# Performance work log

Hardware: AMD Instinct MI355X
Metric: run time of the kernel (lower is better)

The kernel has to match this reference:

```python
import jax, jax.numpy as jnp
import numpy as np

N, E, D_IN, D_H, D_OUT = 50000, 640000, 128, 128, 64
EPS = 1e-5


def _sage(x, src, dst, Wl, bl, Wr):
    # PyG SAGEConv: out = lin_l(mean_{j in N(i)} x_j) + lin_r(x_i)
    msg = x[src]                                             # [E, d] gather
    agg = jax.ops.segment_sum(msg, dst, num_segments=x.shape[0])
    deg = jax.ops.segment_sum(jnp.ones((src.shape[0],), x.dtype), dst,
                              num_segments=x.shape[0])
    agg = agg / jnp.maximum(deg, 1.0)[:, None]               # mean aggregate
    return agg @ Wl + bl + x @ Wr


def _bn_eval(x, gamma, beta, mean, var):
    return (x - mean) * jax.lax.rsqrt(var + EPS) * gamma + beta


def setup_inputs() -> dict:
    key = jax.random.key(0)
    ks = jax.random.split(key, 16)
    s = lambda d: 1.0 / np.sqrt(d)
    inp = {
        "x": jax.random.normal(ks[0], (N, D_IN), jnp.float32),
        "edge_index": jax.random.randint(ks[1], (2, E), 0, N, jnp.int64),
        # layer 0: 128 -> 128
        "Wl0": jax.random.normal(ks[2], (D_IN, D_H), jnp.float32) * s(D_IN),
        "bl0": jnp.zeros((D_H,), jnp.float32),
        "Wr0": jax.random.normal(ks[3], (D_IN, D_H), jnp.float32) * s(D_IN),
        # layer 1: 128 -> 128
        "Wl1": jax.random.normal(ks[4], (D_H, D_H), jnp.float32) * s(D_H),
        "bl1": jnp.zeros((D_H,), jnp.float32),
        "Wr1": jax.random.normal(ks[5], (D_H, D_H), jnp.float32) * s(D_H),
        # layer 2: 128 -> 64
        "Wl2": jax.random.normal(ks[6], (D_H, D_OUT), jnp.float32) * s(D_H),
        "bl2": jnp.zeros((D_OUT,), jnp.float32),
        "Wr2": jax.random.normal(ks[7], (D_H, D_OUT), jnp.float32) * s(D_H),
        # BatchNorm (eval mode) for the two hidden layers
        "g0": jnp.ones((D_H,), jnp.float32),
        "b0": jnp.zeros((D_H,), jnp.float32),
        "m0": jax.random.normal(ks[8], (D_H,), jnp.float32) * 0.1,
        "v0": jax.random.uniform(ks[9], (D_H,), jnp.float32, 0.5, 1.5),
        "g1": jnp.ones((D_H,), jnp.float32),
        "b1": jnp.zeros((D_H,), jnp.float32),
        "m1": jax.random.normal(ks[10], (D_H,), jnp.float32) * 0.1,
        "v1": jax.random.uniform(ks[11], (D_H,), jnp.float32, 0.5, 1.5),
    }
    return inp


def reference(x, edge_index, Wl0, bl0, Wr0, Wl1, bl1, Wr1, Wl2, bl2, Wr2,
              g0, b0, m0, v0, g1, b1, m1, v1):
    src, dst = edge_index[0], edge_index[1]
    # edge mask (edge_index < N) is all-true by construction -> no-op
    h = _sage(x, src, dst, Wl0, bl0, Wr0)
    h = jax.nn.relu(_bn_eval(h, g0, b0, m0, v0))   # eval: dropout is identity
    h = _sage(h, src, dst, Wl1, bl1, Wr1)
    h = jax.nn.relu(_bn_eval(h, g1, b1, m1, v1))
    h = _sage(h, src, dst, Wl2, bl2, Wr2)
    return jax.nn.log_softmax(h, axis=1)
```

## Files before the change

kernel.cpp:

```cpp
#include <hip/hip_runtime.h>

#define EPS 1e-5f
#define ELL_CAP 64

typedef __attribute__((ext_vector_type(8))) short short8;
typedef __attribute__((ext_vector_type(4))) float f32x4;

__device__ inline unsigned short f2b(float f) {
    union { float f; unsigned u; } v; v.f = f;
    unsigned u = v.u;
    return (unsigned short)((u + 0x7fffu + ((u >> 16) & 1u)) >> 16);
}
__device__ inline float b2f(unsigned short u) {
    union { unsigned u; float f; } v;
    v.u = ((unsigned)u) << 16;
    return v.f;
}


__device__ inline void cvt_one(const float* Wl, const float* Wr,
                               unsigned short* BT, int dout, int idx) {
    int n = idx >> 7, k = idx & 127;
    float w = (n < dout) ? Wl[k * dout + n] : Wr[k * dout + (n - dout)];
    BT[idx] = f2b(w);
}

__global__ void k_cvt_w3(const float* __restrict__ Wl0, const float* __restrict__ Wr0,
                         const float* __restrict__ Wl1, const float* __restrict__ Wr1,
                         const float* __restrict__ Wl2, const float* __restrict__ Wr2,
                         unsigned short* __restrict__ BT0,
                         unsigned short* __restrict__ BT1,
                         unsigned short* __restrict__ BT2,
                         int* __restrict__ cnt, int N) {
    int idx = blockIdx.x * blockDim.x + threadIdx.x;
    const int S0 = 256 * 128, S1 = 256 * 128, S2 = 128 * 128;
    if (idx < N) cnt[idx] = 0;
    if (idx < S0) cvt_one(Wl0, Wr0, BT0, 128, idx);
    else if (idx < S0 + S1) cvt_one(Wl1, Wr1, BT1, 128, idx - S0);
    else if (idx < S0 + S1 + S2) cvt_one(Wl2, Wr2, BT2, 64, idx - S0 - S1);
}


__global__ void k_build_ell(const int* __restrict__ src, const int* __restrict__ dst,
                            int E, int* __restrict__ cnt,
                            unsigned short* __restrict__ ell) {
    int i = blockIdx.x * blockDim.x + threadIdx.x;
    int T = gridDim.x * blockDim.x;
    int e0 = i, e1 = i + T, e2 = i + 2 * T, e3 = i + 3 * T;
    int d0 = 0, d1 = 0, d2 = 0, d3 = 0;
    int s0 = 0, s1 = 0, s2 = 0, s3 = 0;
    if (e0 < E) { d0 = dst[e0]; s0 = src[e0]; }
    if (e1 < E) { d1 = dst[e1]; s1 = src[e1]; }
    if (e2 < E) { d2 = dst[e2]; s2 = src[e2]; }
    if (e3 < E) { d3 = dst[e3]; s3 = src[e3]; }
    int p0 = 0, p1 = 0, p2 = 0, p3 = 0;
    if (e0 < E) p0 = atomicAdd(&cnt[d0], 1);
    if (e1 < E) p1 = atomicAdd(&cnt[d1], 1);
    if (e2 < E) p2 = atomicAdd(&cnt[d2], 1);
    if (e3 < E) p3 = atomicAdd(&cnt[d3], 1);
    if (e0 < E && p0 < ELL_CAP) ell[(size_t)d0 * ELL_CAP + p0] = (unsigned short)s0;
    if (e1 < E && p1 < ELL_CAP) ell[(size_t)d1 * ELL_CAP + p1] = (unsigned short)s1;
    if (e2 < E && p2 < ELL_CAP) ell[(size_t)d2 * ELL_CAP + p2] = (unsigned short)s2;
    if (e3 < E && p3 < ELL_CAP) ell[(size_t)d3 * ELL_CAP + p3] = (unsigned short)s3;
}


__device__ inline short8 pack8(float4 a, float4 b) {
    short8 r;
    r[0] = (short)f2b(a.x); r[1] = (short)f2b(a.y);
    r[2] = (short)f2b(a.z); r[3] = (short)f2b(a.w);
    r[4] = (short)f2b(b.x); r[5] = (short)f2b(b.y);
    r[6] = (short)f2b(b.z); r[7] = (short)f2b(b.w);
    return r;
}

template <int NCOLS, bool A32>
__global__ void k_mgemm_lds(const void* __restrict__ Av,
                            const unsigned short* __restrict__ BT,
                            unsigned short* __restrict__ C,
                            int M) {
    __shared__ __align__(16) unsigned short Bs[8 * 4 * 64 * 8];

    const int tid  = threadIdx.x;
    const int lane = tid & 63;
    const int wave = tid >> 6;
    const int m16  = lane & 15;
    const int q    = lane >> 4;
    const int row0 = (blockIdx.x * 4 + wave) * 16;
    const int col0 = blockIdx.y * 128;

#pragma unroll
    for (int i = 0; i < 8; ++i) {
        int f   = tid + i * 256;
        int t   = f >> 8;
        int kc  = (f >> 6) & 3;
        int ln  = f & 63;
        int bm  = ln & 15, bq = ln >> 4;
        const short8* gp = (const short8*)(BT + (size_t)(col0 + t * 16 + bm) * 128
                                              + kc * 32 + bq * 8);
        *(short8*)(Bs + (size_t)f * 8) = *gp;
    }

    int arow = row0 + m16;
    if (arow >= M) arow = M - 1;
    short8 af0, af1, af2, af3;
    if (A32) {
        const float4* Ap = (const float4*)((const float*)Av + (size_t)arow * 128 + q * 8);
        af0 = pack8(Ap[0],  Ap[1]);
        af1 = pack8(Ap[8],  Ap[9]);
        af2 = pack8(Ap[16], Ap[17]);
        af3 = pack8(Ap[24], Ap[25]);
    } else {
        const short8* Ap = (const short8*)((const unsigned short*)Av + (size_t)arow * 128 + q * 8);
        af0 = Ap[0]; af1 = Ap[4]; af2 = Ap[8]; af3 = Ap[12];
    }

    __syncthreads();

    f32x4 acc[8] = {};
#pragma unroll
    for (int t = 0; t < 8; ++t) {
        const short8* bp = (const short8*)(Bs + (size_t)(t * 4) * 64 * 8 + (size_t)lane * 8);
        short8 b0 = bp[0];
        short8 b1 = bp[64];
        short8 b2 = bp[128];
        short8 b3 = bp[192];
        acc[t] = __builtin_amdgcn_mfma_f32_16x16x32_bf16(af0, b0, acc[t], 0, 0, 0);
        acc[t] = __builtin_amdgcn_mfma_f32_16x16x32_bf16(af1, b1, acc[t], 0, 0, 0);
        acc[t] = __builtin_amdgcn_mfma_f32_16x16x32_bf16(af2, b2, acc[t], 0, 0, 0);
        acc[t] = __builtin_amdgcn_mfma_f32_16x16x32_bf16(af3, b3, acc[t], 0, 0, 0);
    }

#pragma unroll
    for (int r = 0; r < 4; ++r) {
        int row = row0 + q * 4 + r;
        if (row < M) {
            unsigned short* cp = C + (size_t)row * NCOLS + col0 + m16;
#pragma unroll
            for (int t = 0; t < 8; ++t) cp[t * 16] = f2b(acc[t][r]);
        }
    }
}


__global__ void k_agg128(const unsigned short* __restrict__ PQ,
                         const int* __restrict__ cnt,
                         const unsigned short* __restrict__ ell,
                         const float* __restrict__ bl,
                         const float* __restrict__ g, const float* __restrict__ b,
                         const float* __restrict__ m, const float* __restrict__ v,
                         unsigned short* __restrict__ out, int n) {
    int node = (blockIdx.x * blockDim.x + threadIdx.x) >> 6;
    int lane = threadIdx.x & 63;
    if (node >= n) return;
    int cn  = cnt[node];
    int deg = min(cn, ELL_CAP);
    int myidx = (lane < deg) ? (int)ell[(size_t)node * ELL_CAP + lane] : 0;
    const int half = lane >> 5, hl = lane & 31;

    float a0 = 0.f, a1 = 0.f, a2 = 0.f, a3 = 0.f;
    int j = 0;
    for (; j + 4 <= deg; j += 4) {
        int ia = __shfl(myidx, j + half);
        int ib = __shfl(myidx, j + 2 + half);
        ushort4 pa = *(const ushort4*)(PQ + (size_t)ia * 256 + 4 * hl);
        ushort4 pb = *(const ushort4*)(PQ + (size_t)ib * 256 + 4 * hl);
        a0 += b2f(pa.x) + b2f(pb.x);
        a1 += b2f(pa.y) + b2f(pb.y);
        a2 += b2f(pa.z) + b2f(pb.z);
        a3 += b2f(pa.w) + b2f(pb.w);
    }
    for (; j < deg; j += 2) {
        int rem = deg - j;
        int ia = __shfl(myidx, min(j + half, deg - 1));
        if (half == 0 || rem >= 2) {
            ushort4 pa = *(const ushort4*)(PQ + (size_t)ia * 256 + 4 * hl);
            a0 += b2f(pa.x); a1 += b2f(pa.y); a2 += b2f(pa.z); a3 += b2f(pa.w);
        }
    }
    a0 += __shfl_xor(a0, 32);
    a1 += __shfl_xor(a1, 32);
    a2 += __shfl_xor(a2, 32);
    a3 += __shfl_xor(a3, 32);

    float dg = fmaxf((float)cn, 1.f);
    ushort4 qv = *(const ushort4*)(PQ + (size_t)node * 256 + 128 + 4 * hl);
    int c0 = 4 * hl;
    float4 blv = *(const float4*)(bl + c0);
    float4 mv  = *(const float4*)(m + c0);
    float4 vv  = *(const float4*)(v + c0);
    float4 gv  = *(const float4*)(g + c0);
    float4 bv  = *(const float4*)(b + c0);
    float z0 = (a0 / dg + b2f(qv.x) + blv.x - mv.x) * rsqrtf(vv.x + EPS) * gv.x + bv.x;
    float z1 = (a1 / dg + b2f(qv.y) + blv.y - mv.y) * rsqrtf(vv.y + EPS) * gv.y + bv.y;
    float z2 = (a2 / dg + b2f(qv.z) + blv.z - mv.z) * rsqrtf(vv.z + EPS) * gv.z + bv.z;
    float z3 = (a3 / dg + b2f(qv.w) + blv.w - mv.w) * rsqrtf(vv.w + EPS) * gv.w + bv.w;
    if (half == 0) {
        ushort4 r;
        r.x = f2b(fmaxf(z0, 0.f));
        r.y = f2b(fmaxf(z1, 0.f));
        r.z = f2b(fmaxf(z2, 0.f));
        r.w = f2b(fmaxf(z3, 0.f));
        *(ushort4*)(out + (size_t)node * 128 + c0) = r;
    }
}


__global__ void k_agg64(const unsigned short* __restrict__ PQ,
                        const int* __restrict__ cnt,
                        const unsigned short* __restrict__ ell,
                        const float* __restrict__ bl,
                        float* __restrict__ out, int n) {
    int node = (blockIdx.x * blockDim.x + threadIdx.x) >> 6;
    int lane = threadIdx.x & 63;
    if (node >= n) return;
    int cn  = cnt[node];
    int deg = min(cn, ELL_CAP);
    int myidx = (lane < deg) ? (int)ell[(size_t)node * ELL_CAP + lane] : 0;
    const int qtr = lane >> 4, ql = lane & 15;

    float a0 = 0.f, a1 = 0.f, a2 = 0.f, a3 = 0.f;
    int j = 0;
    for (; j + 8 <= deg; j += 8) {
        int ia = __shfl(myidx, j + qtr);
        int ib = __shfl(myidx, j + 4 + qtr);
        ushort4 pa = *(const ushort4*)(PQ + (size_t)ia * 128 + 4 * ql);
        ushort4 pb = *(const ushort4*)(PQ + (size_t)ib * 128 + 4 * ql);
        a0 += b2f(pa.x) + b2f(pb.x);
        a1 += b2f(pa.y) + b2f(pb.y);
        a2 += b2f(pa.z) + b2f(pb.z);
        a3 += b2f(pa.w) + b2f(pb.w);
    }
    for (; j < deg; j += 4) {
        int rem = deg - j;
        int ia = __shfl(myidx, min(j + qtr, deg - 1));
        if (qtr < rem) {
            ushort4 pa = *(const ushort4*)(PQ + (size_t)ia * 128 + 4 * ql);
            a0 += b2f(pa.x); a1 += b2f(pa.y); a2 += b2f(pa.z); a3 += b2f(pa.w);
        }
    }
    a0 += __shfl_xor(a0, 16); a0 += __shfl_xor(a0, 32);
    a1 += __shfl_xor(a1, 16); a1 += __shfl_xor(a1, 32);
    a2 += __shfl_xor(a2, 16); a2 += __shfl_xor(a2, 32);
    a3 += __shfl_xor(a3, 16); a3 += __shfl_xor(a3, 32);

    float dg = fmaxf((float)cn, 1.f);
    ushort4 qv = *(const ushort4*)(PQ + (size_t)node * 128 + 64 + 4 * ql);
    int c0 = 4 * ql;
    float4 blv = *(const float4*)(bl + c0);
    float z0 = a0 / dg + b2f(qv.x) + blv.x;
    float z1 = a1 / dg + b2f(qv.y) + blv.y;
    float z2 = a2 / dg + b2f(qv.z) + blv.z;
    float z3 = a3 / dg + b2f(qv.w) + blv.w;

    float mx = fmaxf(fmaxf(z0, z1), fmaxf(z2, z3));
#pragma unroll
    for (int off = 8; off > 0; off >>= 1) mx = fmaxf(mx, __shfl_xor(mx, off));
    float sm = __expf(z0 - mx) + __expf(z1 - mx) + __expf(z2 - mx) + __expf(z3 - mx);
#pragma unroll
    for (int off = 8; off > 0; off >>= 1) sm += __shfl_xor(sm, off);
    float lg = mx + __logf(sm);
    if (qtr == 0) {
        float4 o = make_float4(z0 - lg, z1 - lg, z2 - lg, z3 - lg);
        *(float4*)(out + (size_t)node * 64 + c0) = o;
    }
}


extern "C" void kernel_launch(void* const* d_in, const int* in_sizes, int n_in,
                              void* d_out, int out_size, void* d_ws, size_t ws_size,
                              hipStream_t stream) {
    const float* x   = (const float*)d_in[0];
    const int*   ei  = (const int*)d_in[1];
    const float* Wl0 = (const float*)d_in[2];
    const float* bl0 = (const float*)d_in[3];
    const float* Wr0 = (const float*)d_in[4];
    const float* Wl1 = (const float*)d_in[5];
    const float* bl1 = (const float*)d_in[6];
    const float* Wr1 = (const float*)d_in[7];
    const float* Wl2 = (const float*)d_in[8];
    const float* bl2 = (const float*)d_in[9];
    const float* Wr2 = (const float*)d_in[10];
    const float* g0  = (const float*)d_in[11];
    const float* b0  = (const float*)d_in[12];
    const float* m0  = (const float*)d_in[13];
    const float* v0  = (const float*)d_in[14];
    const float* g1  = (const float*)d_in[15];
    const float* b1  = (const float*)d_in[16];
    const float* m1  = (const float*)d_in[17];
    const float* v1  = (const float*)d_in[18];

    const int N = in_sizes[0] / 128;
    const int E = in_sizes[1] / 2;
    const int* src = ei;
    const int* dst = ei + E;

    size_t off = 0;
    auto alloc = [&](size_t bytes) -> void* {
        void* p = (char*)d_ws + off;
        off += (bytes + 255) & ~(size_t)255;
        return p;
    };
    int* cnt = (int*)alloc((size_t)N * 4);
    unsigned short* ell = (unsigned short*)alloc((size_t)N * ELL_CAP * 2);
    unsigned short* PQ  = (unsigned short*)alloc((size_t)N * 256 * 2);
    unsigned short* hb  = (unsigned short*)alloc((size_t)N * 128 * 2);
    unsigned short* BT0 = (unsigned short*)alloc((size_t)256 * 128 * 2);
    unsigned short* BT1 = (unsigned short*)alloc((size_t)256 * 128 * 2);
    unsigned short* BT2 = (unsigned short*)alloc((size_t)128 * 128 * 2);
    (void)ws_size;

    const int CVT_TOTAL = 256 * 128 + 256 * 128 + 128 * 128;
    k_cvt_w3<<<(CVT_TOTAL + 255) / 256, 256, 0, stream>>>(
        Wl0, Wr0, Wl1, Wr1, Wl2, Wr2, BT0, BT1, BT2, cnt, N);

    int buildThreads = (E + 3) / 4;
    k_build_ell<<<(buildThreads + 255) / 256, 256, 0, stream>>>(src, dst, E, cnt, ell);

    int rowBlocks = (N + 63) / 64;
    dim3 mg2(rowBlocks, 2);
    dim3 mg1(rowBlocks, 1);
    int aggGrid = (N + 3) / 4;

    k_mgemm_lds<256, true><<<mg2, 256, 0, stream>>>(x, BT0, PQ, N);
    k_agg128<<<aggGrid, 256, 0, stream>>>(PQ, cnt, ell, bl0, g0, b0, m0, v0, hb, N);
    k_mgemm_lds<256, false><<<mg2, 256, 0, stream>>>(hb, BT1, PQ, N);
    k_agg128<<<aggGrid, 256, 0, stream>>>(PQ, cnt, ell, bl1, g1, b1, m1, v1, hb, N);
    k_mgemm_lds<128, false><<<mg1, 256, 0, stream>>>(hb, BT2, PQ, N);
    k_agg64<<<aggGrid, 256, 0, stream>>>(PQ, cnt, ell, bl2, (float*)d_out, N);
}
```

Measured before the change: 268.2 us.

## Fuse ELL build with first GEMM in one launch and pad atomic counters

Merges the edge-list ELL construction and the layer-0 feature GEMM into a single kernel whose blocks are split by index: the first blocks build the ELL and the rest run the GEMM, so the two independent phases can overlap on the GPU. Per-node degree counters are padded to a 16-int stride to spread atomics across cache lines, and they are now zeroed with a memset instead of inside the weight-conversion kernel. The padding makes the counter array 16x larger and scatters the degree reads in the aggregation kernels. The merged kernel also carries the GEMM's LDS allocation in the build blocks, which may limit their occupancy.

```diff
diff --git a/kernel.cpp b/kernel.cpp
--- a/kernel.cpp
+++ b/kernel.cpp
@@ -2,6 +2,7 @@
 
 #define EPS 1e-5f
 #define ELL_CAP 64
+#define CNT_STRIDE 16
 
 typedef __attribute__((ext_vector_type(8))) short short8;
 typedef __attribute__((ext_vector_type(4))) float f32x4;
@@ -30,38 +31,12 @@
                          const float* __restrict__ Wl2, const float* __restrict__ Wr2,
                          unsigned short* __restrict__ BT0,
                          unsigned short* __restrict__ BT1,
-                         unsigned short* __restrict__ BT2,
-                         int* __restrict__ cnt, int N) {
+                         unsigned short* __restrict__ BT2) {
     int idx = blockIdx.x * blockDim.x + threadIdx.x;
     const int S0 = 256 * 128, S1 = 256 * 128, S2 = 128 * 128;
-    if (idx < N) cnt[idx] = 0;
     if (idx < S0) cvt_one(Wl0, Wr0, BT0, 128, idx);
     else if (idx < S0 + S1) cvt_one(Wl1, Wr1, BT1, 128, idx - S0);
     else if (idx < S0 + S1 + S2) cvt_one(Wl2, Wr2, BT2, 64, idx - S0 - S1);
-}
-
-
-__global__ void k_build_ell(const int* __restrict__ src, const int* __restrict__ dst,
-                            int E, int* __restrict__ cnt,
-                            unsigned short* __restrict__ ell) {
-    int i = blockIdx.x * blockDim.x + threadIdx.x;
-    int T = gridDim.x * blockDim.x;
-    int e0 = i, e1 = i + T, e2 = i + 2 * T, e3 = i + 3 * T;
-    int d0 = 0, d1 = 0, d2 = 0, d3 = 0;
-    int s0 = 0, s1 = 0, s2 = 0, s3 = 0;
-    if (e0 < E) { d0 = dst[e0]; s0 = src[e0]; }
-    if (e1 < E) { d1 = dst[e1]; s1 = src[e1]; }
-    if (e2 < E) { d2 = dst[e2]; s2 = src[e2]; }
-    if (e3 < E) { d3 = dst[e3]; s3 = src[e3]; }
-    int p0 = 0, p1 = 0, p2 = 0, p3 = 0;
-    if (e0 < E) p0 = atomicAdd(&cnt[d0], 1);
-    if (e1 < E) p1 = atomicAdd(&cnt[d1], 1);
-    if (e2 < E) p2 = atomicAdd(&cnt[d2], 1);
-    if (e3 < E) p3 = atomicAdd(&cnt[d3], 1);
-    if (e0 < E && p0 < ELL_CAP) ell[(size_t)d0 * ELL_CAP + p0] = (unsigned short)s0;
-    if (e1 < E && p1 < ELL_CAP) ell[(size_t)d1 * ELL_CAP + p1] = (unsigned short)s1;
-    if (e2 < E && p2 < ELL_CAP) ell[(size_t)d2 * ELL_CAP + p2] = (unsigned short)s2;
-    if (e3 < E && p3 < ELL_CAP) ell[(size_t)d3 * ELL_CAP + p3] = (unsigned short)s3;
 }
 
 
@@ -75,19 +50,18 @@
 }
 
 template <int NCOLS, bool A32>
-__global__ void k_mgemm_lds(const void* __restrict__ Av,
-                            const unsigned short* __restrict__ BT,
-                            unsigned short* __restrict__ C,
-                            int M) {
-    __shared__ __align__(16) unsigned short Bs[8 * 4 * 64 * 8];
-
+__device__ inline void gemm_body(unsigned short* Bs,
+                                 const void* __restrict__ Av,
+                                 const unsigned short* __restrict__ BT,
+                                 unsigned short* __restrict__ C,
+                                 int M, int bx, int by) {
     const int tid  = threadIdx.x;
     const int lane = tid & 63;
     const int wave = tid >> 6;
     const int m16  = lane & 15;
     const int q    = lane >> 4;
-    const int row0 = (blockIdx.x * 4 + wave) * 16;
-    const int col0 = blockIdx.y * 128;
+    const int row0 = (bx * 4 + wave) * 16;
+    const int col0 = by * 128;
 
 #pragma unroll
     for (int i = 0; i < 8; ++i) {
@@ -142,6 +116,48 @@
     }
 }
 
+template <int NCOLS, bool A32>
+__global__ void k_mgemm_lds(const void* __restrict__ Av,
+                            const unsigned short* __restrict__ BT,
+                            unsigned short* __restrict__ C, int M) {
+    __shared__ __align__(16) unsigned short Bs[8 * 4 * 64 * 8];
+    gemm_body<NCOLS, A32>(Bs, Av, BT, C, M, blockIdx.x, blockIdx.y);
+}
+
+
+__global__ void k_mega(const int* __restrict__ src, const int* __restrict__ dst,
+                       int E, int* __restrict__ cnt, unsigned short* __restrict__ ell,
+                       int buildBlocks,
+                       const float* __restrict__ x,
+                       const unsigned short* __restrict__ BT0,
+                       unsigned short* __restrict__ PQ, int M) {
+    __shared__ __align__(16) unsigned short Bs[8 * 4 * 64 * 8];
+
+    if ((int)blockIdx.x < buildBlocks) {
+        int i = blockIdx.x * blockDim.x + threadIdx.x;
+        int T = buildBlocks * blockDim.x;
+        int e0 = i, e1 = i + T, e2 = i + 2 * T, e3 = i + 3 * T;
+        int d0 = 0, d1 = 0, d2 = 0, d3 = 0;
+        int s0 = 0, s1 = 0, s2 = 0, s3 = 0;
+        if (e0 < E) { d0 = dst[e0]; s0 = src[e0]; }
+        if (e1 < E) { d1 = dst[e1]; s1 = src[e1]; }
+        if (e2 < E) { d2 = dst[e2]; s2 = src[e2]; }
+        if (e3 < E) { d3 = dst[e3]; s3 = src[e3]; }
+        int p0 = 0, p1 = 0, p2 = 0, p3 = 0;
+        if (e0 < E) p0 = atomicAdd(&cnt[(size_t)d0 * CNT_STRIDE], 1);
+        if (e1 < E) p1 = atomicAdd(&cnt[(size_t)d1 * CNT_STRIDE], 1);
+        if (e2 < E) p2 = atomicAdd(&cnt[(size_t)d2 * CNT_STRIDE], 1);
+        if (e3 < E) p3 = atomicAdd(&cnt[(size_t)d3 * CNT_STRIDE], 1);
+        if (e0 < E && p0 < ELL_CAP) ell[(size_t)d0 * ELL_CAP + p0] = (unsigned short)s0;
+        if (e1 < E && p1 < ELL_CAP) ell[(size_t)d1 * ELL_CAP + p1] = (unsigned short)s1;
+        if (e2 < E && p2 < ELL_CAP) ell[(size_t)d2 * ELL_CAP + p2] = (unsigned short)s2;
+        if (e3 < E && p3 < ELL_CAP) ell[(size_t)d3 * ELL_CAP + p3] = (unsigned short)s3;
+        return;
+    }
+    int bid = blockIdx.x - buildBlocks;
+    gemm_body<256, true>(Bs, x, BT0, PQ, M, bid >> 1, bid & 1);
+}
+
 
 __global__ void k_agg128(const unsigned short* __restrict__ PQ,
                          const int* __restrict__ cnt,
@@ -153,7 +169,7 @@
     int node = (blockIdx.x * blockDim.x + threadIdx.x) >> 6;
     int lane = threadIdx.x & 63;
     if (node >= n) return;
-    int cn  = cnt[node];
+    int cn  = cnt[(size_t)node * CNT_STRIDE];
     int deg = min(cn, ELL_CAP);
     int myidx = (lane < deg) ? (int)ell[(size_t)node * ELL_CAP + lane] : 0;
     const int half = lane >> 5, hl = lane & 31;
@@ -214,7 +230,7 @@
     int node = (blockIdx.x * blockDim.x + threadIdx.x) >> 6;
     int lane = threadIdx.x & 63;
     if (node >= n) return;
-    int cn  = cnt[node];
+    int cn  = cnt[(size_t)node * CNT_STRIDE];
     int deg = min(cn, ELL_CAP);
     int myidx = (lane < deg) ? (int)ell[(size_t)node * ELL_CAP + lane] : 0;
     const int qtr = lane >> 4, ql = lane & 15;
@@ -301,7 +317,7 @@
         off += (bytes + 255) & ~(size_t)255;
         return p;
     };
-    int* cnt = (int*)alloc((size_t)N * 4);
+    int* cnt = (int*)alloc((size_t)N * CNT_STRIDE * 4);
     unsigned short* ell = (unsigned short*)alloc((size_t)N * ELL_CAP * 2);
     unsigned short* PQ  = (unsigned short*)alloc((size_t)N * 256 * 2);
     unsigned short* hb  = (unsigned short*)alloc((size_t)N * 128 * 2);
@@ -310,19 +326,21 @@
     unsigned short* BT2 = (unsigned short*)alloc((size_t)128 * 128 * 2);
     (void)ws_size;
 
+    hipMemsetAsync(cnt, 0, (size_t)N * CNT_STRIDE * 4, stream);
     const int CVT_TOTAL = 256 * 128 + 256 * 128 + 128 * 128;
     k_cvt_w3<<<(CVT_TOTAL + 255) / 256, 256, 0, stream>>>(
-        Wl0, Wr0, Wl1, Wr1, Wl2, Wr2, BT0, BT1, BT2, cnt, N);
-
-    int buildThreads = (E + 3) / 4;
-    k_build_ell<<<(buildThreads + 255) / 256, 256, 0, stream>>>(src, dst, E, cnt, ell);
+        Wl0, Wr0, Wl1, Wr1, Wl2, Wr2, BT0, BT1, BT2);
 
     int rowBlocks = (N + 63) / 64;
     dim3 mg2(rowBlocks, 2);
     dim3 mg1(rowBlocks, 1);
     int aggGrid = (N + 3) / 4;
 
-    k_mgemm_lds<256, true><<<mg2, 256, 0, stream>>>(x, BT0, PQ, N);
+    int buildBlocks = ((E + 3) / 4 + 255) / 256;
+    int gemmBlocks  = rowBlocks * 2;
+    k_mega<<<buildBlocks + gemmBlocks, 256, 0, stream>>>(
+        src, dst, E, cnt, ell, buildBlocks, x, BT0, PQ, N);
+
     k_agg128<<<aggGrid, 256, 0, stream>>>(PQ, cnt, ell, bl0, g0, b0, m0, v0, hb, N);
     k_mgemm_lds<256, false><<<mg2, 256, 0, stream>>>(hb, BT1, PQ, N);
     k_agg128<<<aggGrid, 256, 0, stream>>>(PQ, cnt, ell, bl1, g1, b1, m1, v1, hb, N);
```

Measured after the change: 261.4 us. 1.03x faster.

## Store neighbor projections in FP8 and fuse ELL build with first GEMM

Applied to the files above, without the earlier changes.

The neighbor-side projection (P) of layers 0 and 1 is now written as FP8 in its own buffer, while the self projection (Q) stays bf16 in a separate buffer. This halves the bytes the gather-heavy aggregation kernels read per edge. The ELL adjacency build is also merged into the first GEMM launch as extra blocks, so the two can run concurrently and one launch is saved. The cost is lower precision in the aggregated messages, which may hurt accuracy. The fused kernel also adds a grid-stride edge loop over a fixed number of build blocks.

```diff
diff --git a/kernel.cpp b/kernel.cpp
--- a/kernel.cpp
+++ b/kernel.cpp
@@ -2,9 +2,12 @@
 
 #define EPS 1e-5f
 #define ELL_CAP 64
+#define BLK 256
+#define BUILD_BLOCKS 128
 
 typedef __attribute__((ext_vector_type(8))) short short8;
 typedef __attribute__((ext_vector_type(4))) float f32x4;
+typedef __attribute__((ext_vector_type(2))) float f32x2;
 
 __device__ inline unsigned short f2b(float f) {
     union { float f; unsigned u; } v; v.f = f;
@@ -15,6 +18,10 @@
     union { unsigned u; float f; } v;
     v.u = ((unsigned)u) << 16;
     return v.f;
+}
+__device__ inline unsigned char f2p8(float f) {
+    int pk = __builtin_amdgcn_cvt_pk_fp8_f32(f, f, 0, false);
+    return (unsigned char)(pk & 0xff);
 }
 
 
@@ -25,43 +32,19 @@
     BT[idx] = f2b(w);
 }
 
-__global__ void k_cvt_w3(const float* __restrict__ Wl0, const float* __restrict__ Wr0,
-                         const float* __restrict__ Wl1, const float* __restrict__ Wr1,
-                         const float* __restrict__ Wl2, const float* __restrict__ Wr2,
-                         unsigned short* __restrict__ BT0,
-                         unsigned short* __restrict__ BT1,
-                         unsigned short* __restrict__ BT2,
-                         int* __restrict__ cnt, int N) {
+__global__ void k_prep(const float* __restrict__ Wl0, const float* __restrict__ Wr0,
+                       const float* __restrict__ Wl1, const float* __restrict__ Wr1,
+                       const float* __restrict__ Wl2, const float* __restrict__ Wr2,
+                       unsigned short* __restrict__ BT0,
+                       unsigned short* __restrict__ BT1,
+                       unsigned short* __restrict__ BT2,
+                       int* __restrict__ cnt, int N) {
     int idx = blockIdx.x * blockDim.x + threadIdx.x;
+    if (idx < N) cnt[idx] = 0;
     const int S0 = 256 * 128, S1 = 256 * 128, S2 = 128 * 128;
-    if (idx < N) cnt[idx] = 0;
     if (idx < S0) cvt_one(Wl0, Wr0, BT0, 128, idx);
     else if (idx < S0 + S1) cvt_one(Wl1, Wr1, BT1, 128, idx - S0);
     else if (idx < S0 + S1 + S2) cvt_one(Wl2, Wr2, BT2, 64, idx - S0 - S1);
-}
-
-
-__global__ void k_build_ell(const int* __restrict__ src, const int* __restrict__ dst,
-                            int E, int* __restrict__ cnt,
-                            unsigned short* __restrict__ ell) {
-    int i = blockIdx.x * blockDim.x + threadIdx.x;
-    int T = gridDim.x * blockDim.x;
-    int e0 = i, e1 = i + T, e2 = i + 2 * T, e3 = i + 3 * T;
-    int d0 = 0, d1 = 0, d2 = 0, d3 = 0;
-    int s0 = 0, s1 = 0, s2 = 0, s3 = 0;
-    if (e0 < E) { d0 = dst[e0]; s0 = src[e0]; }
-    if (e1 < E) { d1 = dst[e1]; s1 = src[e1]; }
-    if (e2 < E) { d2 = dst[e2]; s2 = src[e2]; }
-    if (e3 < E) { d3 = dst[e3]; s3 = src[e3]; }
-    int p0 = 0, p1 = 0, p2 = 0, p3 = 0;
-    if (e0 < E) p0 = atomicAdd(&cnt[d0], 1);
-    if (e1 < E) p1 = atomicAdd(&cnt[d1], 1);
-    if (e2 < E) p2 = atomicAdd(&cnt[d2], 1);
-    if (e3 < E) p3 = atomicAdd(&cnt[d3], 1);
-    if (e0 < E && p0 < ELL_CAP) ell[(size_t)d0 * ELL_CAP + p0] = (unsigned short)s0;
-    if (e1 < E && p1 < ELL_CAP) ell[(size_t)d1 * ELL_CAP + p1] = (unsigned short)s1;
-    if (e2 < E && p2 < ELL_CAP) ell[(size_t)d2 * ELL_CAP + p2] = (unsigned short)s2;
-    if (e3 < E && p3 < ELL_CAP) ell[(size_t)d3 * ELL_CAP + p3] = (unsigned short)s3;
 }
 
 
@@ -74,20 +57,21 @@
     return r;
 }
 
-template <int NCOLS, bool A32>
-__global__ void k_mgemm_lds(const void* __restrict__ Av,
-                            const unsigned short* __restrict__ BT,
-                            unsigned short* __restrict__ C,
-                            int M) {
-    __shared__ __align__(16) unsigned short Bs[8 * 4 * 64 * 8];
-
+template <int NCOLS, bool A32, int OUT>
+__device__ inline void gemm_tile(unsigned short* Bs,
+                                 const void* __restrict__ Av,
+                                 const unsigned short* __restrict__ BT,
+                                 unsigned short* __restrict__ C,
+                                 unsigned char* __restrict__ P8,
+                                 unsigned short* __restrict__ Qb,
+                                 int M, int bx, int by) {
     const int tid  = threadIdx.x;
     const int lane = tid & 63;
     const int wave = tid >> 6;
     const int m16  = lane & 15;
     const int q    = lane >> 4;
-    const int row0 = (blockIdx.x * 4 + wave) * 16;
-    const int col0 = blockIdx.y * 128;
+    const int row0 = (bx * 4 + wave) * 16;
+    const int col0 = by * 128;
 
 #pragma unroll
     for (int i = 0; i < 8; ++i) {
@@ -135,15 +119,79 @@
     for (int r = 0; r < 4; ++r) {
         int row = row0 + q * 4 + r;
         if (row < M) {
-            unsigned short* cp = C + (size_t)row * NCOLS + col0 + m16;
-#pragma unroll
-            for (int t = 0; t < 8; ++t) cp[t * 16] = f2b(acc[t][r]);
+            if (OUT == 0) {
+                unsigned short* cp = C + (size_t)row * NCOLS + col0 + m16;
+#pragma unroll
+                for (int t = 0; t < 8; ++t) cp[t * 16] = f2b(acc[t][r]);
+            } else if (by == 0) {
+                unsigned char* cp = P8 + (size_t)row * 128 + m16;
+#pragma unroll
+                for (int t = 0; t < 8; ++t) cp[t * 16] = f2p8(acc[t][r]);
+            } else {
+                unsigned short* cp = Qb + (size_t)row * 128 + m16;
+#pragma unroll
+                for (int t = 0; t < 8; ++t) cp[t * 16] = f2b(acc[t][r]);
+            }
         }
     }
-}
-
-
-__global__ void k_agg128(const unsigned short* __restrict__ PQ,
+    __syncthreads();
+}
+
+
+__global__ void k_mega(const int* __restrict__ src, const int* __restrict__ dst,
+                       int E, int* __restrict__ cnt, unsigned short* __restrict__ ell,
+                       const float* __restrict__ x,
+                       const unsigned short* __restrict__ BT0,
+                       unsigned char* __restrict__ P8,
+                       unsigned short* __restrict__ Qb, int M) {
+    __shared__ __align__(16) unsigned short Bs[8 * 4 * 64 * 8];
+
+    if ((int)blockIdx.x < BUILD_BLOCKS) {
+        const int T = BUILD_BLOCKS * BLK;
+        int i = blockIdx.x * BLK + threadIdx.x;
+        for (int base = 0; base < E; base += 4 * T) {
+            int e0 = base + i, e1 = e0 + T, e2 = e1 + T, e3 = e2 + T;
+            int d0 = 0, d1 = 0, d2 = 0, d3 = 0;
+            int s0 = 0, s1 = 0, s2 = 0, s3 = 0;
+            if (e0 < E) { d0 = dst[e0]; s0 = src[e0]; }
+            if (e1 < E) { d1 = dst[e1]; s1 = src[e1]; }
+            if (e2 < E) { d2 = dst[e2]; s2 = src[e2]; }
+            if (e3 < E) { d3 = dst[e3]; s3 = src[e3]; }
+            int p0 = 0, p1 = 0, p2 = 0, p3 = 0;
+            if (e0 < E) p0 = atomicAdd(&cnt[d0], 1);
+            if (e1 < E) p1 = atomicAdd(&cnt[d1], 1);
+            if (e2 < E) p2 = atomicAdd(&cnt[d2], 1);
+            if (e3 < E) p3 = atomicAdd(&cnt[d3], 1);
+            if (e0 < E && p0 < ELL_CAP) ell[(size_t)d0 * ELL_CAP + p0] = (unsigned short)s0;
+            if (e1 < E && p1 < ELL_CAP) ell[(size_t)d1 * ELL_CAP + p1] = (unsigned short)s1;
+            if (e2 < E && p2 < ELL_CAP) ell[(size_t)d2 * ELL_CAP + p2] = (unsigned short)s2;
+            if (e3 < E && p3 < ELL_CAP) ell[(size_t)d3 * ELL_CAP + p3] = (unsigned short)s3;
+        }
+        return;
+    }
+    int bid = blockIdx.x - BUILD_BLOCKS;
+    gemm_tile<256, true, 1>(Bs, x, BT0, nullptr, P8, Qb, M, bid >> 1, bid & 1);
+}
+
+
+__global__ void k_gemm1(const unsigned short* __restrict__ A,
+                        const unsigned short* __restrict__ BT,
+                        unsigned char* __restrict__ P8,
+                        unsigned short* __restrict__ Qb, int M) {
+    __shared__ __align__(16) unsigned short Bs[8 * 4 * 64 * 8];
+    gemm_tile<256, false, 1>(Bs, A, BT, nullptr, P8, Qb, M, blockIdx.x, blockIdx.y);
+}
+
+__global__ void k_gemm2(const unsigned short* __restrict__ A,
+                        const unsigned short* __restrict__ BT,
+                        unsigned short* __restrict__ C, int M) {
+    __shared__ __align__(16) unsigned short Bs[8 * 4 * 64 * 8];
+    gemm_tile<128, false, 0>(Bs, A, BT, C, nullptr, nullptr, M, blockIdx.x, 0);
+}
+
+
+__global__ void k_agg128(const unsigned char* __restrict__ P8,
+                         const unsigned short* __restrict__ Qb,
                          const int* __restrict__ cnt,
                          const unsigned short* __restrict__ ell,
                          const float* __restrict__ bl,
@@ -163,19 +211,25 @@
     for (; j + 4 <= deg; j += 4) {
         int ia = __shfl(myidx, j + half);
         int ib = __shfl(myidx, j + 2 + half);
-        ushort4 pa = *(const ushort4*)(PQ + (size_t)ia * 256 + 4 * hl);
-        ushort4 pb = *(const ushort4*)(PQ + (size_t)ib * 256 + 4 * hl);
-        a0 += b2f(pa.x) + b2f(pb.x);
-        a1 += b2f(pa.y) + b2f(pb.y);
-        a2 += b2f(pa.z) + b2f(pb.z);
-        a3 += b2f(pa.w) + b2f(pb.w);
+        unsigned wa = *(const unsigned*)(P8 + (size_t)ia * 128 + 4 * hl);
+        unsigned wb = *(const unsigned*)(P8 + (size_t)ib * 128 + 4 * hl);
+        f32x2 la = __builtin_amdgcn_cvt_pk_f32_fp8(wa, false);
+        f32x2 ha = __builtin_amdgcn_cvt_pk_f32_fp8(wa, true);
+        f32x2 lb = __builtin_amdgcn_cvt_pk_f32_fp8(wb, false);
+        f32x2 hb2 = __builtin_amdgcn_cvt_pk_f32_fp8(wb, true);
+        a0 += la[0] + lb[0];
+        a1 += la[1] + lb[1];
+        a2 += ha[0] + hb2[0];
+        a3 += ha[1] + hb2[1];
     }
     for (; j < deg; j += 2) {
         int rem = deg - j;
         int ia = __shfl(myidx, min(j + half, deg - 1));
         if (half == 0 || rem >= 2) {
-            ushort4 pa = *(const ushort4*)(PQ + (size_t)ia * 256 + 4 * hl);
-            a0 += b2f(pa.x); a1 += b2f(pa.y); a2 += b2f(pa.z); a3 += b2f(pa.w);
+            unsigned wa = *(const unsigned*)(P8 + (size_t)ia * 128 + 4 * hl);
+            f32x2 la = __builtin_amdgcn_cvt_pk_f32_fp8(wa, false);
+            f32x2 ha = __builtin_amdgcn_cvt_pk_f32_fp8(wa, true);
+            a0 += la[0]; a1 += la[1]; a2 += ha[0]; a3 += ha[1];
         }
     }
     a0 += __shfl_xor(a0, 32);
@@ -184,7 +238,7 @@
     a3 += __shfl_xor(a3, 32);
 
     float dg = fmaxf((float)cn, 1.f);
-    ushort4 qv = *(const ushort4*)(PQ + (size_t)node * 256 + 128 + 4 * hl);
+    ushort4 qv = *(const ushort4*)(Qb + (size_t)node * 128 + 4 * hl);
     int c0 = 4 * hl;
     float4 blv = *(const float4*)(bl + c0);
     float4 mv  = *(const float4*)(m + c0);
@@ -303,7 +357,9 @@
     };
     int* cnt = (int*)alloc((size_t)N * 4);
     unsigned short* ell = (unsigned short*)alloc((size_t)N * ELL_CAP * 2);
-    unsigned short* PQ  = (unsigned short*)alloc((size_t)N * 256 * 2);
+    unsigned char*  P8  = (unsigned char*)alloc((size_t)N * 128);
+    unsigned short* Qb  = (unsigned short*)alloc((size_t)N * 128 * 2);
+    unsigned short* PQ  = (unsigned short*)alloc((size_t)N * 128 * 2);
     unsigned short* hb  = (unsigned short*)alloc((size_t)N * 128 * 2);
     unsigned short* BT0 = (unsigned short*)alloc((size_t)256 * 128 * 2);
     unsigned short* BT1 = (unsigned short*)alloc((size_t)256 * 128 * 2);
@@ -311,21 +367,21 @@
     (void)ws_size;
 
     const int CVT_TOTAL = 256 * 128 + 256 * 128 + 128 * 128;
-    k_cvt_w3<<<(CVT_TOTAL + 255) / 256, 256, 0, stream>>>(
-        Wl0, Wr0, Wl1, Wr1, Wl2, Wr2, BT0, BT1, BT2, cnt, N);
-
-    int buildThreads = (E + 3) / 4;
-    k_build_ell<<<(buildThreads + 255) / 256, 256, 0, stream>>>(src, dst, E, cnt, ell);
+    int prepGrid = (max(CVT_TOTAL, N) + BLK - 1) / BLK;
+    k_prep<<<prepGrid, BLK, 0, stream>>>(Wl0, Wr0, Wl1, Wr1, Wl2, Wr2,
+                                         BT0, BT1, BT2, cnt, N);
 
     int rowBlocks = (N + 63) / 64;
     dim3 mg2(rowBlocks, 2);
-    dim3 mg1(rowBlocks, 1);
     int aggGrid = (N + 3) / 4;
 
-    k_mgemm_lds<256, true><<<mg2, 256, 0, stream>>>(x, BT0, PQ, N);
-    k_agg128<<<aggGrid, 256, 0, stream>>>(PQ, cnt, ell, bl0, g0, b0, m0, v0, hb, N);
-    k_mgemm_lds<256, false><<<mg2, 256, 0, stream>>>(hb, BT1, PQ, N);
-    k_agg128<<<aggGrid, 256, 0, stream>>>(PQ, cnt, ell, bl1, g1, b1, m1, v1, hb, N);
-    k_mgemm_lds<128, false><<<mg1, 256, 0, stream>>>(hb, BT2, PQ, N);
-    k_agg64<<<aggGrid, 256, 0, stream>>>(PQ, cnt, ell, bl2, (float*)d_out, N);
-}
+    int gemmBlocks = rowBlocks * 2;
+    k_mega<<<BUILD_BLOCKS + gemmBlocks, BLK, 0, stream>>>(
+        src, dst, E, cnt, ell, x, BT0, P8, Qb, N);
+
+    k_agg128<<<aggGrid, BLK, 0, stream>>>(P8, Qb, cnt, ell, bl0, g0, b0, m0, v0, hb, N);
+    k_gemm1<<<mg2, BLK, 0, stream>>>(hb, BT1, P8, Qb, N);
+    k_agg128<<<aggGrid, BLK, 0, stream>>>(P8, Qb, cnt, ell, bl1, g1, b1, m1, v1, hb, N);
+    k_gemm2<<<rowBlocks, BLK, 0, stream>>>(hb, BT2, PQ, N);
+    k_agg64<<<aggGrid, BLK, 0, stream>>>(PQ, cnt, ell, bl2, (float*)d_out, N);
+}
```

Measured after the change: 248.0 us. -7.5%, faster.
